# Kernel optimization log

Hardware: AMD Instinct MI355X
Metric: run time of the kernel (lower is better)

Reference implementation:

```python
import jax, jax.numpy as jnp
import numpy as np

N_SPINS = 128
GAMMA = 0.25
T_MF = 25
DAMPING = 0.7
TOL = 1e-4
BATCH = 262144


def setup_inputs() -> dict:
    key = jax.random.key(0)
    k1, k2, k3 = jax.random.split(key, 3)
    features = jax.random.normal(k1, (BATCH, N_SPINS), dtype=jnp.float32)
    local_field = jax.random.normal(k2, (N_SPINS,), dtype=jnp.float32) * 0.1
    interaction_matrix = jax.random.normal(k3, (N_SPINS, N_SPINS), dtype=jnp.float32) * (0.1 / np.sqrt(N_SPINS))
    return {"features": features, "local_field": local_field, "interaction_matrix": interaction_matrix}


def reference(features, local_field, interaction_matrix):
    # mask zeroes the diagonal of J (registered buffer in torch)
    mask = 1.0 - jnp.eye(N_SPINS, dtype=features.dtype)
    Jm = interaction_matrix * mask  # [S,S]

    spins0 = jnp.tanh(features[:, :N_SPINS] * 0.1)  # [B,S]

    def body(carry, t):
        spins, done = carry
        h_eff = local_field + spins @ Jm                      # [B,S]
        new = jnp.tanh(h_eff / GAMMA)                         # [B,S]
        upd = DAMPING * new + (1.0 - DAMPING) * spins         # damped update
        spins_next = jnp.where(done, spins, upd)              # freeze after early-exit
        # torch: break if t>5 and ||new_spins - expected_spins|| < tol (post-update diff)
        hit = (t > 5) & (jnp.linalg.norm(new - upd) < TOL)
        return (spins_next, done | hit), None

    (spins, _), _ = jax.lax.scan(body, (spins0, jnp.array(False)), jnp.arange(T_MF))

    h_final = local_field + spins @ Jm
    free_energy = -GAMMA * jnp.sum(jnp.log(2.0 * jnp.cosh(h_final / GAMMA)), axis=-1, keepdims=True)  # [B,1]
    return (spins, free_energy)
```

## Files before the change

kernel.cpp:

```cpp
#include <hip/hip_runtime.h>
#include <hip/hip_bf16.h>
#include <stdint.h>

typedef float f32x4 __attribute__((ext_vector_type(4)));
typedef short short8 __attribute__((ext_vector_type(8)));

#define LDSPAD 136
#define C8 11.54156509f

static __device__ __forceinline__ unsigned short f2bf(float f) {
    union { float f; uint32_t u; } x; x.f = f;
    return (unsigned short)((x.u + 0x7FFFu + ((x.u >> 16) & 1u)) >> 16);
}
static __device__ __forceinline__ uint32_t pk2(float a, float b) {
    float2 t; t.x = a; t.y = b;
    union { __hip_bfloat162 h; uint32_t u; } c;
    c.h = __float22bfloat162_rn(t);
    return c.u;
}
static __device__ __forceinline__ float tanh_e2(float arg) {
    float E = __builtin_amdgcn_exp2f(arg);
    return __builtin_fmaf(-2.0f, __builtin_amdgcn_rcpf(E + 1.0f), 1.0f);
}

__global__ __launch_bounds__(256, 2)
void mf_ising(const float* __restrict__ feat, const float* __restrict__ lf,
              const float* __restrict__ Jg, float* __restrict__ out) {
    __shared__ __align__(16) unsigned short LB[128 * LDSPAD];

    const int tid  = threadIdx.x;
    const int wave = tid >> 6;
    const int lane = tid & 63;
    const int j    = lane & 15;
    const int g    = lane >> 4;

    #pragma unroll 4
    for (int c = 0; c < 64; ++c) {
        int flat = c * 256 + tid;
        int k = flat >> 7, i = flat & 127;
        float v = (i == k) ? 0.0f : Jg[flat];
        LB[i * LDSPAD + k] = f2bf(v);
    }
    __syncthreads();

    short8 aFr[8][4];
    #pragma unroll
    for (int it = 0; it < 8; ++it)
        #pragma unroll
        for (int kt = 0; kt < 4; ++kt)
            aFr[it][kt] = *(const short8*)&LB[(16 * it + j) * LDSPAD + 32 * kt + 8 * g];
    __syncthreads();

    const int rowBase = blockIdx.x * 64 + wave * 16;
    unsigned short* SL = &LB[(wave * 16) * LDSPAD];

    f32x4 lfv[8];
    #pragma unroll
    for (int it = 0; it < 8; ++it)
        lfv[it] = *(const f32x4*)(lf + it * 16 + g * 4);

    f32x4 sreg[8];
    {
        const size_t row = (size_t)(rowBase + j);
        #pragma unroll
        for (int it = 0; it < 8; ++it) {
            f32x4 fv = *(const f32x4*)(feat + row * 128 + it * 16 + g * 4);
            f32x4 s;
            #pragma unroll
            for (int r = 0; r < 4; ++r) s[r] = tanh_e2(0.28853901f * fv[r]);
            sreg[it] = s;
        }
    }

    f32x4 acc[8];

    auto matvec = [&]() {
        unsigned short* srow = &SL[j * LDSPAD];
        #pragma unroll
        for (int it = 0; it < 8; ++it) {
            uint2 v;
            v.x = pk2(sreg[it][0], sreg[it][1]);
            v.y = pk2(sreg[it][2], sreg[it][3]);
            *(uint2*)(srow + it * 16 + g * 4) = v;
        }
        #pragma unroll
        for (int kt = 0; kt < 4; ++kt) {
            short8 b = *(const short8*)&SL[j * LDSPAD + kt * 32 + g * 8];
            if (kt == 0) {
                #pragma unroll
                for (int it = 0; it < 8; ++it)
                    acc[it] = __builtin_amdgcn_mfma_f32_16x16x32_bf16(aFr[it][0], b, lfv[it], 0, 0, 0);
            } else {
                #pragma unroll
                for (int it = 0; it < 8; ++it)
                    acc[it] = __builtin_amdgcn_mfma_f32_16x16x32_bf16(aFr[it][kt], b, acc[it], 0, 0, 0);
            }
        }
    };

    #pragma unroll 1
    for (int t = 0; t < 25; ++t) {
        matvec();
        #pragma unroll
        for (int it = 0; it < 8; ++it) {
            f32x4 s = sreg[it], h = acc[it];
            #pragma unroll
            for (int r = 0; r < 4; ++r) {
                float E = __builtin_amdgcn_exp2f(h[r] * C8);
                float rc = __builtin_amdgcn_rcpf(E + 1.0f);
                s[r] = __builtin_fmaf(-1.4f, rc, __builtin_fmaf(0.3f, s[r], 0.7f));
            }
            sreg[it] = s;
        }
    }
    matvec();

    {
        const size_t row = (size_t)(rowBase + j);
        #pragma unroll
        for (int it = 0; it < 8; ++it)
            *(f32x4*)(out + row * 128 + it * 16 + g * 4) = sreg[it];
    }
    float p = 0.0f;
    #pragma unroll
    for (int it = 0; it < 8; ++it) {
        #pragma unroll
        for (int r = 0; r < 4; ++r) {
            float y = 4.0f * acc[it][r];
            float a = fabsf(y);
            float q = __builtin_amdgcn_exp2f(-2.88539008f * a);
            p += a + 0.69314718f * __builtin_amdgcn_logf(1.0f + q);
        }
    }
    p += __shfl_xor(p, 16, 64);
    p += __shfl_xor(p, 32, 64);
    if (lane < 16) {
        size_t row = (size_t)(rowBase + j);
        out[(size_t)262144 * 128 + row] = -0.25f * p;
    }
}

extern "C" void kernel_launch(void* const* d_in, const int* in_sizes, int n_in,
                              void* d_out, int out_size, void* d_ws, size_t ws_size,
                              hipStream_t stream) {
    const float* feat = (const float*)d_in[0];
    const float* lfld = (const float*)d_in[1];
    const float* Jg   = (const float*)d_in[2];
    float* out = (float*)d_out;
    (void)in_sizes; (void)n_in; (void)out_size; (void)d_ws; (void)ws_size;

    dim3 grid(262144 / 64), block(256);
    hipLaunchKernelGGL(mf_ising, grid, block, 0, stream, feat, lfld, Jg, out);
}
```

Before: 509.6 us.

## Process two row tiles per wave with J held in swizzled LDS

Each wave now handles 32 batch rows (two 16-row tiles) instead of 16, and the grid is halved. The J fragments are no longer cached in registers. They are reloaded from a transposed, XOR-swizzled LDS copy each k-step and reused across both row tiles. The padded layout is replaced by XOR swizzling for both J and the spin staging buffer, which avoids bank conflicts. This frees registers for the doubled accumulators, but adds LDS A-fragment reads to every iteration and uses 64KB of LDS per block, which may limit occupancy.

```diff
diff --git a/kernel.cpp b/kernel.cpp
--- a/kernel.cpp
+++ b/kernel.cpp
@@ -5,8 +5,7 @@
 typedef float f32x4 __attribute__((ext_vector_type(4)));
 typedef short short8 __attribute__((ext_vector_type(8)));
 
-#define LDSPAD 136
-#define C8 11.54156509f
+#define C8 11.5415603f
 
 static __device__ __forceinline__ unsigned short f2bf(float f) {
     union { float f; uint32_t u; } x; x.f = f;
@@ -26,74 +25,80 @@
 __global__ __launch_bounds__(256, 2)
 void mf_ising(const float* __restrict__ feat, const float* __restrict__ lf,
               const float* __restrict__ Jg, float* __restrict__ out) {
-    __shared__ __align__(16) unsigned short LB[128 * LDSPAD];
+    __shared__ __align__(16) unsigned short JT[128 * 128];
+    __shared__ __align__(16) unsigned short SL[128 * 128];
 
     const int tid  = threadIdx.x;
     const int wave = tid >> 6;
     const int lane = tid & 63;
     const int j    = lane & 15;
     const int g    = lane >> 4;
+    const int sw   = (j & 7) << 4;
 
-    #pragma unroll 4
-    for (int c = 0; c < 64; ++c) {
-        int flat = c * 256 + tid;
-        int k = flat >> 7, i = flat & 127;
-        float v = (i == k) ? 0.0f : Jg[flat];
-        LB[i * LDSPAD + k] = f2bf(v);
+    {
+        const int il = lane & 15, kl = lane >> 4;
+        const int ibase = wave * 32 + il;
+        #pragma unroll 4
+        for (int c = 0; c < 64; ++c) {
+            int i = ibase + 16 * (c & 1);
+            int k = kl + 4 * (c >> 1);
+            float v = (i == k) ? 0.0f : Jg[k * 128 + i];
+            JT[i * 128 + (((2 * k) ^ ((i & 7) << 4)) >> 1)] = f2bf(v);
+        }
     }
     __syncthreads();
 
-    short8 aFr[8][4];
-    #pragma unroll
-    for (int it = 0; it < 8; ++it)
-        #pragma unroll
-        for (int kt = 0; kt < 4; ++kt)
-            aFr[it][kt] = *(const short8*)&LB[(16 * it + j) * LDSPAD + 32 * kt + 8 * g];
-    __syncthreads();
-
-    const int rowBase = blockIdx.x * 64 + wave * 16;
-    unsigned short* SL = &LB[(wave * 16) * LDSPAD];
+    const int rowBase = blockIdx.x * 128 + wave * 32;
+    const int slRow   = wave * 32 + j;
 
     f32x4 lfv[8];
     #pragma unroll
     for (int it = 0; it < 8; ++it)
         lfv[it] = *(const f32x4*)(lf + it * 16 + g * 4);
 
-    f32x4 sreg[8];
-    {
-        const size_t row = (size_t)(rowBase + j);
+    f32x4 sreg[2][8];
+    #pragma unroll
+    for (int jt = 0; jt < 2; ++jt) {
+        const size_t row = (size_t)(rowBase + jt * 16 + j);
         #pragma unroll
         for (int it = 0; it < 8; ++it) {
             f32x4 fv = *(const f32x4*)(feat + row * 128 + it * 16 + g * 4);
             f32x4 s;
             #pragma unroll
             for (int r = 0; r < 4; ++r) s[r] = tanh_e2(0.28853901f * fv[r]);
-            sreg[it] = s;
+            sreg[jt][it] = s;
         }
     }
 
-    f32x4 acc[8];
+    f32x4 acc[2][8];
 
     auto matvec = [&]() {
-        unsigned short* srow = &SL[j * LDSPAD];
         #pragma unroll
-        for (int it = 0; it < 8; ++it) {
-            uint2 v;
-            v.x = pk2(sreg[it][0], sreg[it][1]);
-            v.y = pk2(sreg[it][2], sreg[it][3]);
-            *(uint2*)(srow + it * 16 + g * 4) = v;
+        for (int jt = 0; jt < 2; ++jt) {
+            unsigned short* srow = &SL[(slRow + jt * 16) * 128];
+            #pragma unroll
+            for (int it = 0; it < 8; ++it) {
+                uint2 v;
+                v.x = pk2(sreg[jt][it][0], sreg[jt][it][1]);
+                v.y = pk2(sreg[jt][it][2], sreg[jt][it][3]);
+                *(uint2*)(srow + (((it * 32 + g * 8) ^ sw) >> 1)) = v;
+            }
         }
         #pragma unroll
         for (int kt = 0; kt < 4; ++kt) {
-            short8 b = *(const short8*)&SL[j * LDSPAD + kt * 32 + g * 8];
-            if (kt == 0) {
-                #pragma unroll
-                for (int it = 0; it < 8; ++it)
-                    acc[it] = __builtin_amdgcn_mfma_f32_16x16x32_bf16(aFr[it][0], b, lfv[it], 0, 0, 0);
-            } else {
-                #pragma unroll
-                for (int it = 0; it < 8; ++it)
-                    acc[it] = __builtin_amdgcn_mfma_f32_16x16x32_bf16(aFr[it][kt], b, acc[it], 0, 0, 0);
+            const int ro = ((kt * 64 + g * 16) ^ sw) >> 1;
+            short8 b0 = *(const short8*)&SL[(slRow)      * 128 + ro];
+            short8 b1 = *(const short8*)&SL[(slRow + 16) * 128 + ro];
+            #pragma unroll
+            for (int it = 0; it < 8; ++it) {
+                short8 a = *(const short8*)&JT[(16 * it + j) * 128 + ro];
+                if (kt == 0) {
+                    acc[0][it] = __builtin_amdgcn_mfma_f32_16x16x32_bf16(a, b0, lfv[it], 0, 0, 0);
+                    acc[1][it] = __builtin_amdgcn_mfma_f32_16x16x32_bf16(a, b1, lfv[it], 0, 0, 0);
+                } else {
+                    acc[0][it] = __builtin_amdgcn_mfma_f32_16x16x32_bf16(a, b0, acc[0][it], 0, 0, 0);
+                    acc[1][it] = __builtin_amdgcn_mfma_f32_16x16x32_bf16(a, b1, acc[1][it], 0, 0, 0);
+                }
             }
         }
     };
@@ -102,41 +107,48 @@
     for (int t = 0; t < 25; ++t) {
         matvec();
         #pragma unroll
-        for (int it = 0; it < 8; ++it) {
-            f32x4 s = sreg[it], h = acc[it];
+        for (int jt = 0; jt < 2; ++jt) {
             #pragma unroll
-            for (int r = 0; r < 4; ++r) {
-                float E = __builtin_amdgcn_exp2f(h[r] * C8);
-                float rc = __builtin_amdgcn_rcpf(E + 1.0f);
-                s[r] = __builtin_fmaf(-1.4f, rc, __builtin_fmaf(0.3f, s[r], 0.7f));
+            for (int it = 0; it < 8; ++it) {
+                f32x4 s = sreg[jt][it], h = acc[jt][it];
+                #pragma unroll
+                for (int r = 0; r < 4; ++r) {
+                    float E  = __builtin_amdgcn_exp2f(h[r] * C8);
+                    float rc = __builtin_amdgcn_rcpf(E + 1.0f);
+                    s[r] = __builtin_fmaf(-1.4f, rc, __builtin_fmaf(0.3f, s[r], 0.7f));
+                }
+                sreg[jt][it] = s;
             }
-            sreg[it] = s;
         }
     }
     matvec();
 
-    {
-        const size_t row = (size_t)(rowBase + j);
+    #pragma unroll
+    for (int jt = 0; jt < 2; ++jt) {
+        const size_t row = (size_t)(rowBase + jt * 16 + j);
         #pragma unroll
         for (int it = 0; it < 8; ++it)
-            *(f32x4*)(out + row * 128 + it * 16 + g * 4) = sreg[it];
+            *(f32x4*)(out + row * 128 + it * 16 + g * 4) = sreg[jt][it];
     }
-    float p = 0.0f;
     #pragma unroll
-    for (int it = 0; it < 8; ++it) {
+    for (int jt = 0; jt < 2; ++jt) {
+        float p = 0.0f;
         #pragma unroll
-        for (int r = 0; r < 4; ++r) {
-            float y = 4.0f * acc[it][r];
-            float a = fabsf(y);
-            float q = __builtin_amdgcn_exp2f(-2.88539008f * a);
-            p += a + 0.69314718f * __builtin_amdgcn_logf(1.0f + q);
+        for (int it = 0; it < 8; ++it) {
+            #pragma unroll
+            for (int r = 0; r < 4; ++r) {
+                float y = 4.0f * acc[jt][it][r];
+                float a = fabsf(y);
+                float q = __builtin_amdgcn_exp2f(-2.88539008f * a);
+                p += a + 0.69314718f * __builtin_amdgcn_logf(1.0f + q);
+            }
         }
-    }
-    p += __shfl_xor(p, 16, 64);
-    p += __shfl_xor(p, 32, 64);
-    if (lane < 16) {
-        size_t row = (size_t)(rowBase + j);
-        out[(size_t)262144 * 128 + row] = -0.25f * p;
+        p += __shfl_xor(p, 16, 64);
+        p += __shfl_xor(p, 32, 64);
+        if (lane < 16) {
+            size_t row = (size_t)(rowBase + jt * 16 + j);
+            out[(size_t)262144 * 128 + row] = -0.25f * p;
+        }
     }
 }
 
@@ -149,6 +161,6 @@
     float* out = (float*)d_out;
     (void)in_sizes; (void)n_in; (void)out_size; (void)d_ws; (void)ws_size;
 
-    dim3 grid(262144 / 64), block(256);
+    dim3 grid(2048), block(256);
     hipLaunchKernelGGL(mf_ising, grid, block, 0, stream, feat, lfld, Jg, out);
 }
```

New measurement: 900.5 us. 76.7% more time.
